# Kernel tuning notes

Measured on AMD Instinct MI355X. Metric: run time of the kernel, lower is better.

## Reference

```python
import jax, jax.numpy as jnp
import numpy as np

N = 16_777_216  # total samples in batch
S = 1024        # number of distinct stations/basins
EPS = 1e-6


def setup_inputs() -> dict:
    key = jax.random.key(0)
    k1, k2, k3, k4 = jax.random.split(key, 4)
    y_pred = jax.random.normal(k1, (N,), dtype=jnp.float32)
    y_true = jax.random.normal(k2, (N,), dtype=jnp.float32)
    stations = jax.random.randint(k3, (N,), 0, S, dtype=jnp.int32)
    # per-station observed-discharge std (kept away from 0 for realism)
    station_std = jax.random.uniform(k4, (S,), dtype=jnp.float32) + 0.5
    return {"y_pred": y_pred, "y_true": y_true, "stations": stations,
            "station_std": station_std}


def reference(y_pred, y_true, stations, station_std):
    y_pred = y_pred.reshape(-1)
    y_true = y_true.reshape(-1)
    err2 = (y_pred - y_true) ** 2                                   # [N]
    sse = jax.ops.segment_sum(err2, stations, num_segments=S)       # [S]
    cnt = jax.ops.segment_sum(jnp.ones_like(err2), stations, num_segments=S)
    mse = sse / jnp.maximum(cnt, 1.0)                                # per-station MSE
    denom = (station_std + EPS) ** 2                                 # (sigma+eps)^2
    present = cnt > 0                                                # stations in batch
    per_station = jnp.where(present, mse / denom, 0.0)
    n_present = jnp.maximum(jnp.sum(present.astype(jnp.float32)), 1.0)
    return jnp.sum(per_station) / n_present
```

## Files before the change

kernel.cpp:

```cpp
#include <hip/hip_runtime.h>

#define NUM_S 1024
constexpr float EPS = 1e-6f;

constexpr unsigned CNT_ONE_32 = 1u << 25;
constexpr unsigned SSE_MASK_32 = (1u << 25) - 1;
constexpr int CNT_SHIFT_64 = 44;
constexpr unsigned long long SSE_MASK_64 = (1ULL << 44) - 1;
constexpr float FP_SCALE = 4096.0f;
constexpr double FP_INV_SCALE = 1.0 / 4096.0;

__global__ __launch_bounds__(1024, 2) void nse_partial_kernel(
    const float4* __restrict__ yp4, const float4* __restrict__ yt4,
    const int4* __restrict__ st4, const float* __restrict__ yp,
    const float* __restrict__ yt, const int* __restrict__ st,
    unsigned long long* __restrict__ g_hist, int n, int n4)
{
    __shared__ unsigned s_hist[NUM_S];
    for (int i = threadIdx.x; i < NUM_S; i += blockDim.x) {
        s_hist[i] = 0u;
    }
    __syncthreads();

    const int gtid = blockIdx.x * blockDim.x + threadIdx.x;
    const int stride = gridDim.x * blockDim.x;

    for (int i = gtid; i < n4; i += stride) {
        float4 p = yp4[i];
        float4 t = yt4[i];
        int4 s = st4[i];
        float dx = p.x - t.x;
        float dy = p.y - t.y;
        float dz = p.z - t.z;
        float dw = p.w - t.w;
        unsigned fx = (unsigned)(dx * dx * FP_SCALE + 0.5f);
        unsigned fy = (unsigned)(dy * dy * FP_SCALE + 0.5f);
        unsigned fz = (unsigned)(dz * dz * FP_SCALE + 0.5f);
        unsigned fw = (unsigned)(dw * dw * FP_SCALE + 0.5f);
        atomicAdd(&s_hist[s.x], CNT_ONE_32 | fx);
        atomicAdd(&s_hist[s.y], CNT_ONE_32 | fy);
        atomicAdd(&s_hist[s.z], CNT_ONE_32 | fz);
        atomicAdd(&s_hist[s.w], CNT_ONE_32 | fw);
    }
    for (int i = n4 * 4 + gtid; i < n; i += stride) {
        float d = yp[i] - yt[i];
        unsigned f = (unsigned)(d * d * FP_SCALE + 0.5f);
        atomicAdd(&s_hist[st[i]], CNT_ONE_32 | f);
    }
    __syncthreads();

    for (int i = threadIdx.x; i < NUM_S; i += blockDim.x) {
        unsigned h = s_hist[i];
        if (h != 0u) {
            unsigned long long packed =
                ((unsigned long long)(h >> 25) << CNT_SHIFT_64) |
                (unsigned long long)(h & SSE_MASK_32);
            atomicAdd(&g_hist[i], packed);
        }
    }
}

__global__ __launch_bounds__(1024) void nse_final_kernel(
    const unsigned long long* __restrict__ g_hist,
    const float* __restrict__ station_std, float* __restrict__ out)
{
    const int s = threadIdx.x;
    unsigned long long h = g_hist[s];
    float c = (float)(unsigned)(h >> CNT_SHIFT_64);
    float v = (float)((double)(h & SSE_MASK_64) * FP_INV_SCALE);
    float sd = station_std[s];
    float denom = (sd + EPS) * (sd + EPS);
    float per = (c > 0.0f) ? (v / fmaxf(c, 1.0f)) / denom : 0.0f;
    float pres = (c > 0.0f) ? 1.0f : 0.0f;

    #pragma unroll
    for (int o = 32; o > 0; o >>= 1) {
        per += __shfl_down(per, o, 64);
        pres += __shfl_down(pres, o, 64);
    }

    __shared__ float w_per[16];
    __shared__ float w_pres[16];
    const int lane = threadIdx.x & 63;
    const int wid = threadIdx.x >> 6;
    if (lane == 0) {
        w_per[wid] = per;
        w_pres[wid] = pres;
    }
    __syncthreads();

    if (wid == 0) {
        float sp = (lane < 16) ? w_per[lane] : 0.0f;
        float sc = (lane < 16) ? w_pres[lane] : 0.0f;
        #pragma unroll
        for (int o = 8; o > 0; o >>= 1) {
            sp += __shfl_down(sp, o, 64);
            sc += __shfl_down(sc, o, 64);
        }
        if (lane == 0) {
            out[0] = sp / fmaxf(sc, 1.0f);
        }
    }
}

extern "C" void kernel_launch(void* const* d_in, const int* in_sizes, int n_in,
                              void* d_out, int out_size, void* d_ws, size_t ws_size,
                              hipStream_t stream) {
    const float* y_pred = (const float*)d_in[0];
    const float* y_true = (const float*)d_in[1];
    const int* stations = (const int*)d_in[2];
    const float* station_std = (const float*)d_in[3];
    float* out = (float*)d_out;

    const int n = in_sizes[0];
    const int n4 = n / 4;

    unsigned long long* g_hist = (unsigned long long*)d_ws;

    hipMemsetAsync(d_ws, 0, NUM_S * sizeof(unsigned long long), stream);

    dim3 grid(512);
    dim3 block(1024);
    nse_partial_kernel<<<grid, block, 0, stream>>>(
        (const float4*)y_pred, (const float4*)y_true, (const int4*)stations,
        y_pred, y_true, stations, g_hist, n, n4);

    nse_final_kernel<<<1, 1024, 0, stream>>>(g_hist, station_std, out);
}
```

Baseline: 199.8 us.

## Use per-wave LDS histograms with ballot-based match to replace shared atomics

Each wave gets a private 1024-bin LDS histogram. Lanes targeting the same station are detected by ten ballots over the station bits and serialized by rank, so updates become plain read-modify-writes instead of LDS atomics. The per-wave histograms are summed per bin before the global atomic flush. This aims to remove atomic contention and serialization, at the cost of many extra ballot/ALU instructions per element and 16x more LDS, which may cut occupancy.

```diff
diff --git a/kernel.cpp b/kernel.cpp
--- a/kernel.cpp
+++ b/kernel.cpp
@@ -1,8 +1,9 @@
 #include <hip/hip_runtime.h>
 
 #define NUM_S 1024
+#define NWAVE 16
+
 constexpr float EPS = 1e-6f;
-
 constexpr unsigned CNT_ONE_32 = 1u << 25;
 constexpr unsigned SSE_MASK_32 = (1u << 25) - 1;
 constexpr int CNT_SHIFT_64 = 44;
@@ -10,14 +11,35 @@
 constexpr float FP_SCALE = 4096.0f;
 constexpr double FP_INV_SCALE = 1.0 / 4096.0;
 
+__device__ __forceinline__ void accum_one(unsigned* __restrict__ whist,
+                                          unsigned s, unsigned contrib) {
+    unsigned long long mask = ~0ULL;
+    #pragma unroll
+    for (int b = 0; b < 10; ++b) {
+        unsigned long long bal = __ballot((s >> b) & 1u);
+        mask &= ((s >> b) & 1u) ? bal : ~bal;
+    }
+    unsigned rank = __builtin_amdgcn_mbcnt_lo((unsigned)mask, 0u);
+    rank = __builtin_amdgcn_mbcnt_hi((unsigned)(mask >> 32), rank);
+    for (unsigned r = 0;; ++r) {
+        if (!__any(rank == r)) break;
+        if (rank == r) {
+            whist[s] += contrib;
+        }
+    }
+}
+
 __global__ __launch_bounds__(1024, 2) void nse_partial_kernel(
     const float4* __restrict__ yp4, const float4* __restrict__ yt4,
     const int4* __restrict__ st4, const float* __restrict__ yp,
     const float* __restrict__ yt, const int* __restrict__ st,
     unsigned long long* __restrict__ g_hist, int n, int n4)
 {
-    __shared__ unsigned s_hist[NUM_S];
-    for (int i = threadIdx.x; i < NUM_S; i += blockDim.x) {
+    __shared__ unsigned s_hist[NWAVE * NUM_S];
+    const int wid = threadIdx.x >> 6;
+    unsigned* whist = s_hist + wid * NUM_S;
+
+    for (int i = threadIdx.x; i < NWAVE * NUM_S; i += blockDim.x) {
         s_hist[i] = 0u;
     }
     __syncthreads();
@@ -37,24 +59,31 @@
         unsigned fy = (unsigned)(dy * dy * FP_SCALE + 0.5f);
         unsigned fz = (unsigned)(dz * dz * FP_SCALE + 0.5f);
         unsigned fw = (unsigned)(dw * dw * FP_SCALE + 0.5f);
-        atomicAdd(&s_hist[s.x], CNT_ONE_32 | fx);
-        atomicAdd(&s_hist[s.y], CNT_ONE_32 | fy);
-        atomicAdd(&s_hist[s.z], CNT_ONE_32 | fz);
-        atomicAdd(&s_hist[s.w], CNT_ONE_32 | fw);
+        accum_one(whist, (unsigned)s.x, CNT_ONE_32 | fx);
+        accum_one(whist, (unsigned)s.y, CNT_ONE_32 | fy);
+        accum_one(whist, (unsigned)s.z, CNT_ONE_32 | fz);
+        accum_one(whist, (unsigned)s.w, CNT_ONE_32 | fw);
     }
     for (int i = n4 * 4 + gtid; i < n; i += stride) {
         float d = yp[i] - yt[i];
         unsigned f = (unsigned)(d * d * FP_SCALE + 0.5f);
-        atomicAdd(&s_hist[st[i]], CNT_ONE_32 | f);
+        atomicAdd(&whist[st[i]], CNT_ONE_32 | f);
     }
     __syncthreads();
 
     for (int i = threadIdx.x; i < NUM_S; i += blockDim.x) {
-        unsigned h = s_hist[i];
-        if (h != 0u) {
+        unsigned cnt_sum = 0u;
+        unsigned sse_sum = 0u;
+        #pragma unroll
+        for (int w = 0; w < NWAVE; ++w) {
+            unsigned h = s_hist[w * NUM_S + i];
+            cnt_sum += h >> 25;
+            sse_sum += h & SSE_MASK_32;
+        }
+        if (cnt_sum != 0u) {
             unsigned long long packed =
-                ((unsigned long long)(h >> 25) << CNT_SHIFT_64) |
-                (unsigned long long)(h & SSE_MASK_32);
+                ((unsigned long long)cnt_sum << CNT_SHIFT_64) |
+                (unsigned long long)sse_sum;
             atomicAdd(&g_hist[i], packed);
         }
     }
```

Result: slower. 205.7 us (+2.9%).
